# Kernel optimization log

Measured on AMD Instinct MI355X. Metric: run time of the kernel, lower is better.

The kernel has to match this reference:

```python
import jax, jax.numpy as jnp
import numpy as np

C = 64
C2 = C // 2


def conv1x1(x, w, b):
    # x: [B,Cin,H,W], w: [Cout,Cin], b: [Cout]
    return jnp.einsum('bchw,oc->bohw', x, w) + b[None, :, None, None]


def maxpool2(x):
    # 2x2 max pool, stride 2. x: [B,C,H,W] -> [B,C,H//2,W//2]
    B, Ch, H, W = x.shape
    x = x.reshape(B, Ch, H // 2, 2, W // 2, 2)
    return x.max(axis=(3, 5))


def setup_inputs() -> dict:
    key = jax.random.key(0)
    ks = jax.random.split(key, 9)
    B, H, W = 4, 128, 128
    x = jax.random.normal(ks[0], (B, C, H, W), dtype=jnp.float32)
    s_in = 1.0 / np.sqrt(C)
    s_mid = 1.0 / np.sqrt(C2)
    return {
        'x': x,
        'w_theta': jax.random.uniform(ks[1], (C2, C), jnp.float32, -s_in, s_in),
        'b_theta': jax.random.uniform(ks[2], (C2,), jnp.float32, -s_in, s_in),
        'w_phi': jax.random.uniform(ks[3], (C2, C), jnp.float32, -s_in, s_in),
        'b_phi': jax.random.uniform(ks[4], (C2,), jnp.float32, -s_in, s_in),
        'w_g': jax.random.uniform(ks[5], (C2, C), jnp.float32, -s_in, s_in),
        'b_g': jax.random.uniform(ks[6], (C2,), jnp.float32, -s_in, s_in),
        'w_out': jax.random.uniform(ks[7], (C, C2), jnp.float32, -s_mid, s_mid),
        'b_out': jax.random.uniform(ks[8], (C,), jnp.float32, -s_mid, s_mid),
    }


def reference(x, w_theta, b_theta, w_phi, b_phi, w_g, b_g, w_out, b_out):
    B, Ch, H, W = x.shape
    theta = conv1x1(x, w_theta, b_theta)            # [B,C2,H,W]
    phi = maxpool2(conv1x1(x, w_phi, b_phi))        # [B,C2,H/2,W/2]
    g = maxpool2(conv1x1(x, w_g, b_g))              # [B,C2,H/2,W/2]

    theta_flat = theta.reshape(B, C2, H * W).transpose(0, 2, 1)   # [B,HW,C2]
    phi_flat = phi.reshape(B, C2, -1)                              # [B,C2,hw4]
    g_flat = g.reshape(B, C2, -1).transpose(0, 2, 1)               # [B,hw4,C2]

    attn = jnp.einsum('bnc,bcm->bnm', theta_flat, phi_flat)       # [B,HW,hw4]
    attn = jax.nn.softmax(attn, axis=-1)
    y = jnp.einsum('bnm,bmc->bnc', attn, g_flat)                   # [B,HW,C2]
    y = y.transpose(0, 2, 1).reshape(B, C2, H, W)
    return conv1x1(y, w_out, b_out) + x
```

## Files before the change

kernel.cpp:

```cpp
#include <hip/hip_runtime.h>

#define HW    16384
#define Wh    128
#define Cin   64
#define C2    32
#define HW4   4096

typedef short short8 __attribute__((ext_vector_type(8)));
typedef float float4v __attribute__((ext_vector_type(4)));
typedef unsigned uint4v __attribute__((ext_vector_type(4)));

#define LOG2E 1.44269504f
#define OFFE  43.2808512f

__device__ __forceinline__ unsigned pack2bf16(float lo, float hi) {
  unsigned ul = __builtin_bit_cast(unsigned, lo);
  unsigned uh = __builtin_bit_cast(unsigned, hi);
  ul = (ul + 0x7fffu + ((ul >> 16) & 1u)) >> 16;
  uh = (uh + 0x7fffu + ((uh >> 16) & 1u)) & 0xffff0000u;
  return ul | uh;
}
__device__ __forceinline__ unsigned short f2bf(float f) {
  unsigned u = __builtin_bit_cast(unsigned, f);
  return (unsigned short)((u + 0x7fffu + ((u >> 16) & 1u)) >> 16);
}
__device__ __forceinline__ unsigned packtrunc(float lo, float hi) {
  return __builtin_amdgcn_perm(__builtin_bit_cast(unsigned, hi),
                               __builtin_bit_cast(unsigned, lo), 0x07060302u);
}

__global__ __launch_bounds__(256) void repack_w_kern(
    const float* __restrict__ wt, const float* __restrict__ bt,
    const float* __restrict__ wp, const float* __restrict__ bp,
    const float* __restrict__ wg, const float* __restrict__ bg,
    float* __restrict__ wAll, float* __restrict__ bAll) {
  int idx = blockIdx.x * 256 + threadIdx.x;
  if (idx < 6144) {
    int og = idx / 1536, rem = idx % 1536;
    int c = rem / 24, j = rem % 24;
    int o = og * 8 + (j & 7);
    float v;
    if (j < 8)       v = wt[o * Cin + c] * LOG2E;
    else if (j < 16) v = wp[o * Cin + c];
    else             v = wg[o * Cin + c];
    wAll[idx] = v;
  } else if (idx < 6240) {
    int i2 = idx - 6144;
    int og = i2 / 24, j = i2 % 24;
    int o = og * 8 + (j & 7);
    bAll[i2] = (j < 8) ? bt[o] * LOG2E : (j < 16 ? bp[o] : bg[o]);
  }
}

__global__ __launch_bounds__(256) void conv_qkv_kern(
    const float* __restrict__ x, const float* __restrict__ wAll,
    const float* __restrict__ bAll, unsigned short* __restrict__ Q,
    unsigned short* __restrict__ K, unsigned short* __restrict__ Vt) {
  __shared__ float smX[2][8][256];
  __shared__ unsigned short smV[8][64];
  int tid = threadIdx.x;
  int og = blockIdx.y, bz = blockIdx.z;
  int pxbase = blockIdx.x * 2 * Wh;
  int jloc = tid >> 2;
  int rpar = (tid >> 1) & 1, cpar = tid & 1;
  int myPx = rpar * Wh + 2 * jloc + cpar;
  const float* xb = x + (size_t)bz * Cin * HW + pxbase;
  const float* wc = wAll + og * 1536;
  const float* bb = bAll + og * 24;

  auto stage = [&](int cb8, int buf) {
#pragma unroll
    for (int u = 0; u < 2; ++u) {
      int f = u * 256 + tid;
      int ch = f >> 6, p4 = f & 63;
      *(float4*)&smX[buf][ch][p4 * 4] =
          *(const float4*)(xb + (size_t)(cb8 * 8 + ch) * HW + p4 * 4);
    }
  };

  float acc[24];
#pragma unroll
  for (int k = 0; k < 24; ++k) acc[k] = bb[k];

  stage(0, 0);
  __syncthreads();
  for (int cb8 = 0; cb8 < 8; ++cb8) {
    if (cb8 < 7) stage(cb8 + 1, (cb8 + 1) & 1);
    float xv[8];
#pragma unroll
    for (int u = 0; u < 8; ++u) xv[u] = smX[cb8 & 1][u][myPx];
#pragma unroll
    for (int u = 0; u < 8; ++u) {
#pragma unroll
      for (int k = 0; k < 24; ++k)
        acc[k] = fmaf(wc[(cb8 * 8 + u) * 24 + k], xv[u], acc[k]);
    }
    __syncthreads();
  }

  int pp = blockIdx.x * 64 + jloc;
  int p = pxbase + myPx;
  {
    uint4 up;
    up.x = pack2bf16(acc[0], acc[1]); up.y = pack2bf16(acc[2], acc[3]);
    up.z = pack2bf16(acc[4], acc[5]); up.w = pack2bf16(acc[6], acc[7]);
    *(uint4*)(Q + ((size_t)bz * HW + p) * C2 + og * 8) = up;
  }
  float aP[8], aG[8];
#pragma unroll
  for (int o = 0; o < 8; ++o) {
    float vp = acc[8 + o], vg = acc[16 + o];
    vp = fmaxf(vp, __shfl_xor(vp, 1)); vp = fmaxf(vp, __shfl_xor(vp, 2));
    vg = fmaxf(vg, __shfl_xor(vg, 1)); vg = fmaxf(vg, __shfl_xor(vg, 2));
    aP[o] = vp; aG[o] = vg;
  }
  if ((tid & 3) == 0) {
    int loc = pp & 31, tile = pp >> 5;
    int prow = ((loc & 4) << 2) + ((loc >> 3) << 2) + (loc & 3);
    uint4 up;
    up.x = pack2bf16(aP[0], aP[1]); up.y = pack2bf16(aP[2], aP[3]);
    up.z = pack2bf16(aP[4], aP[5]); up.w = pack2bf16(aP[6], aP[7]);
    *(uint4*)(K + ((size_t)bz * HW4 + tile * 32 + prow) * C2 + og * 8) = up;
#pragma unroll
    for (int o = 0; o < 8; ++o) smV[o][tid >> 2] = f2bf(aG[o]);
  }
  __syncthreads();
  {
    int ch = tid >> 5, idx = tid & 31;
    unsigned v = ((unsigned*)smV)[ch * 32 + idx];
    int tile = blockIdx.x * 2 + (idx >> 4);
    int kin = (2 * idx) & 31;
    *(unsigned*)(Vt + (size_t)bz * C2 * HW4 + (size_t)tile * (C2 * 32) +
                 (size_t)(og * 8 + ch) * 32 + kin) = v;
  }
}

__global__ __launch_bounds__(256, 4) void attn_mfma_kern(
    const unsigned short* __restrict__ Qb, const unsigned short* __restrict__ Kb,
    const unsigned short* __restrict__ Vt, float* __restrict__ Y) {
  __shared__ float smY[3][64][33];
  __shared__ float smL[4][64];
  int lane = threadIdx.x & 63;
  int wv = threadIdx.x >> 6;
  int quad = lane >> 4, l16 = lane & 15;
  int bz = blockIdx.y;
  int qrow0 = blockIdx.x * 64;

  short8 qf[4];
#pragma unroll
  for (int f = 0; f < 4; ++f)
    qf[f] = *(const short8*)(Qb + ((size_t)bz * HW + qrow0 + f * 16 + l16) * C2 + quad * 8);
  const unsigned short* kb = Kb + ((size_t)bz * HW4 + wv * 1024) * C2;
  const unsigned short* vb = Vt + (size_t)bz * C2 * HW4 + (size_t)(wv * 32) * 1024;

  short8 ones;
#pragma unroll
  for (int i = 0; i < 8; ++i) ones[i] = (short)0x3F80;

  float4v z = {0.f, 0.f, 0.f, 0.f};
  float4v ya[4] = {z, z, z, z};
  float4v yh[4] = {z, z, z, z};
  float4v y2[4] = {z, z, z, z};
  float4v moff = {-OFFE, -OFFE, -OFFE, -OFFE};

  for (int t = 0; t < 32; ++t) {
    const unsigned short* kt = kb + (size_t)t * 32 * C2;
    const unsigned short* vt = vb + (size_t)t * 1024;
    short8 ka = *(const short8*)(kt + (size_t)l16 * C2 + quad * 8);
    short8 kh = *(const short8*)(kt + (size_t)(16 + l16) * C2 + quad * 8);
    short8 va = *(const short8*)(vt + l16 * 32 + quad * 8);
    short8 vh = *(const short8*)(vt + (16 + l16) * 32 + quad * 8);
#pragma unroll
    for (int f = 0; f < 4; ++f) {
      float4v sa = __builtin_amdgcn_mfma_f32_16x16x32_bf16(ka, qf[f], moff, 0, 0, 0);
      float4v sh = __builtin_amdgcn_mfma_f32_16x16x32_bf16(kh, qf[f], moff, 0, 0, 0);
      float e0 = __builtin_amdgcn_exp2f(sa[0]), e1 = __builtin_amdgcn_exp2f(sa[1]);
      float e2 = __builtin_amdgcn_exp2f(sa[2]), e3 = __builtin_amdgcn_exp2f(sa[3]);
      float g0 = __builtin_amdgcn_exp2f(sh[0]), g1 = __builtin_amdgcn_exp2f(sh[1]);
      float g2 = __builtin_amdgcn_exp2f(sh[2]), g3 = __builtin_amdgcn_exp2f(sh[3]);
      uint4v d = {packtrunc(e0, e1), packtrunc(e2, e3),
                  packtrunc(g0, g1), packtrunc(g2, g3)};
      short8 pf = __builtin_bit_cast(short8, d);
      ya[f] = __builtin_amdgcn_mfma_f32_16x16x32_bf16(pf, va,   ya[f], 0, 0, 0);
      yh[f] = __builtin_amdgcn_mfma_f32_16x16x32_bf16(pf, vh,   yh[f], 0, 0, 0);
      y2[f] = __builtin_amdgcn_mfma_f32_16x16x32_bf16(pf, ones, y2[f], 0, 0, 0);
    }
  }

  if (l16 == 0) {
#pragma unroll
    for (int f = 0; f < 4; ++f)
#pragma unroll
      for (int r = 0; r < 4; ++r)
        smL[wv][f * 16 + quad * 4 + r] = y2[f][r];
  }
  if (wv > 0) {
    int pi = wv - 1;
#pragma unroll
    for (int f = 0; f < 4; ++f)
#pragma unroll
      for (int r = 0; r < 4; ++r) {
        int lr = f * 16 + quad * 4 + r;
        smY[pi][lr][l16] = ya[f][r];
        smY[pi][lr][16 + l16] = yh[f][r];
      }
  }
  __syncthreads();
  if (wv == 0) {
#pragma unroll
    for (int f = 0; f < 4; ++f)
#pragma unroll
      for (int r = 0; r < 4; ++r) {
        int lr = f * 16 + quad * 4 + r;
        float a0 = ya[f][r] + smY[0][lr][l16] + smY[1][lr][l16] + smY[2][lr][l16];
        float a1 = yh[f][r] + smY[0][lr][16 + l16] + smY[1][lr][16 + l16] + smY[2][lr][16 + l16];
        float L = smL[0][lr] + smL[1][lr] + smL[2][lr] + smL[3][lr];
        float inv = 1.f / L;
        size_t rw = (size_t)bz * HW + qrow0 + lr;
        Y[rw * C2 + l16] = a0 * inv;
        Y[rw * C2 + 16 + l16] = a1 * inv;
      }
  }
}

__global__ __launch_bounds__(256) void conv_out_kern(
    const float* __restrict__ Y, const float* __restrict__ x,
    const float* __restrict__ w, const float* __restrict__ bias,
    float* __restrict__ out) {
  int p = blockIdx.x * 256 + threadIdx.x;
  int cog = blockIdx.y, bz = blockIdx.z;
  const float* xb = x + (size_t)bz * Cin * HW + p;
  float xr[8];
#pragma unroll
  for (int i = 0; i < 8; ++i)
    xr[i] = xb[(size_t)(cog * 8 + i) * HW];
  float y[C2];
  const float4* yp4 = (const float4*)(Y + ((size_t)bz * HW + p) * C2);
#pragma unroll
  for (int i = 0; i < 8; ++i) {
    float4 t = yp4[i];
    y[4 * i] = t.x; y[4 * i + 1] = t.y; y[4 * i + 2] = t.z; y[4 * i + 3] = t.w;
  }
  float* ob = out + (size_t)bz * Cin * HW + p;
#pragma unroll
  for (int i = 0; i < 8; ++i) {
    int co = cog * 8 + i;
    float s = bias[co];
#pragma unroll
    for (int o = 0; o < C2; ++o) s = fmaf(w[co * C2 + o], y[o], s);
    ob[(size_t)co * HW] = s + xr[i];
  }
}

extern "C" void kernel_launch(void* const* d_in, const int* in_sizes, int n_in,
                              void* d_out, int out_size, void* d_ws, size_t ws_size,
                              hipStream_t stream) {
  const float* x       = (const float*)d_in[0];
  const float* w_theta = (const float*)d_in[1];
  const float* b_theta = (const float*)d_in[2];
  const float* w_phi   = (const float*)d_in[3];
  const float* b_phi   = (const float*)d_in[4];
  const float* w_g     = (const float*)d_in[5];
  const float* b_g     = (const float*)d_in[6];
  const float* w_out   = (const float*)d_in[7];
  const float* b_out   = (const float*)d_in[8];
  float* out = (float*)d_out;

  float* Yws = (float*)d_ws;
  unsigned short* Qb = (unsigned short*)(Yws + (size_t)4 * HW * C2);
  unsigned short* Kb = Qb + (size_t)4 * HW * C2;
  unsigned short* Vt = Kb + (size_t)4 * HW4 * C2;
  float* wAll = (float*)(Vt + (size_t)4 * HW4 * C2);
  float* bAll = wAll + 6144;

  repack_w_kern<<<25, 256, 0, stream>>>(w_theta, b_theta, w_phi, b_phi,
                                        w_g, b_g, wAll, bAll);
  conv_qkv_kern<<<dim3(64, 4, 4), 256, 0, stream>>>(x, wAll, bAll, Qb, Kb, Vt);
  attn_mfma_kern<<<dim3(HW / 64, 4), 256, 0, stream>>>(Qb, Kb, Vt, Yws);
  conv_out_kern<<<dim3(64, 8, 4), 256, 0, stream>>>(Yws, x, w_out, b_out, out);
}
```

Before: 152.2 us.

## Split attention key range across 8 waves with tree reduction

The attention kernel now launches 512 threads per block, so 8 waves each process 512 keys instead of 4 waves each processing 1024. This halves each wave's serial loop length and adds more waves per CU to hide MFMA and exp latency. Partial outputs are combined with a three-stage shared-memory tree reduction. The cost is extra barriers and LDS traffic, plus register pressure under the launch bound of 512 threads with 4 blocks.

```diff
diff --git a/kernel.cpp b/kernel.cpp
--- a/kernel.cpp
+++ b/kernel.cpp
@@ -135,11 +135,11 @@
   }
 }
 
-__global__ __launch_bounds__(256, 4) void attn_mfma_kern(
+__global__ __launch_bounds__(512, 4) void attn_mfma_kern(
     const unsigned short* __restrict__ Qb, const unsigned short* __restrict__ Kb,
     const unsigned short* __restrict__ Vt, float* __restrict__ Y) {
-  __shared__ float smY[3][64][33];
-  __shared__ float smL[4][64];
+  __shared__ float smY[4][64][33];
+  __shared__ float smL[8][64];
   int lane = threadIdx.x & 63;
   int wv = threadIdx.x >> 6;
   int quad = lane >> 4, l16 = lane & 15;
@@ -150,8 +150,8 @@
 #pragma unroll
   for (int f = 0; f < 4; ++f)
     qf[f] = *(const short8*)(Qb + ((size_t)bz * HW + qrow0 + f * 16 + l16) * C2 + quad * 8);
-  const unsigned short* kb = Kb + ((size_t)bz * HW4 + wv * 1024) * C2;
-  const unsigned short* vb = Vt + (size_t)bz * C2 * HW4 + (size_t)(wv * 32) * 1024;
+  const unsigned short* kb = Kb + ((size_t)bz * HW4 + wv * 512) * C2;
+  const unsigned short* vb = Vt + (size_t)bz * C2 * HW4 + (size_t)(wv * 16) * 1024;
 
   short8 ones;
 #pragma unroll
@@ -163,7 +163,7 @@
   float4v y2[4] = {z, z, z, z};
   float4v moff = {-OFFE, -OFFE, -OFFE, -OFFE};
 
-  for (int t = 0; t < 32; ++t) {
+  for (int t = 0; t < 16; ++t) {
     const unsigned short* kt = kb + (size_t)t * 32 * C2;
     const unsigned short* vt = vb + (size_t)t * 1024;
     short8 ka = *(const short8*)(kt + (size_t)l16 * C2 + quad * 8);
@@ -194,15 +194,58 @@
       for (int r = 0; r < 4; ++r)
         smL[wv][f * 16 + quad * 4 + r] = y2[f][r];
   }
-  if (wv > 0) {
-    int pi = wv - 1;
-#pragma unroll
-    for (int f = 0; f < 4; ++f)
-#pragma unroll
-      for (int r = 0; r < 4; ++r) {
-        int lr = f * 16 + quad * 4 + r;
-        smY[pi][lr][l16] = ya[f][r];
-        smY[pi][lr][16 + l16] = yh[f][r];
+  if (wv >= 4) {
+#pragma unroll
+    for (int f = 0; f < 4; ++f)
+#pragma unroll
+      for (int r = 0; r < 4; ++r) {
+        int lr = f * 16 + quad * 4 + r;
+        smY[wv - 4][lr][l16] = ya[f][r];
+        smY[wv - 4][lr][16 + l16] = yh[f][r];
+      }
+  }
+  __syncthreads();
+  if (wv < 4) {
+#pragma unroll
+    for (int f = 0; f < 4; ++f)
+#pragma unroll
+      for (int r = 0; r < 4; ++r) {
+        int lr = f * 16 + quad * 4 + r;
+        ya[f][r] += smY[wv][lr][l16];
+        yh[f][r] += smY[wv][lr][16 + l16];
+      }
+  }
+  __syncthreads();
+  if (wv == 2 || wv == 3) {
+#pragma unroll
+    for (int f = 0; f < 4; ++f)
+#pragma unroll
+      for (int r = 0; r < 4; ++r) {
+        int lr = f * 16 + quad * 4 + r;
+        smY[wv - 2][lr][l16] = ya[f][r];
+        smY[wv - 2][lr][16 + l16] = yh[f][r];
+      }
+  }
+  __syncthreads();
+  if (wv < 2) {
+#pragma unroll
+    for (int f = 0; f < 4; ++f)
+#pragma unroll
+      for (int r = 0; r < 4; ++r) {
+        int lr = f * 16 + quad * 4 + r;
+        ya[f][r] += smY[wv][lr][l16];
+        yh[f][r] += smY[wv][lr][16 + l16];
+      }
+  }
+  __syncthreads();
+  if (wv == 1) {
+#pragma unroll
+    for (int f = 0; f < 4; ++f)
+#pragma unroll
+      for (int r = 0; r < 4; ++r) {
+        int lr = f * 16 + quad * 4 + r;
+        smY[0][lr][l16] = ya[f][r];
+        smY[0][lr][16 + l16] = yh[f][r];
       }
   }
   __syncthreads();
@@ -212,9 +255,10 @@
 #pragma unroll
       for (int r = 0; r < 4; ++r) {
         int lr = f * 16 + quad * 4 + r;
-        float a0 = ya[f][r] + smY[0][lr][l16] + smY[1][lr][l16] + smY[2][lr][l16];
-        float a1 = yh[f][r] + smY[0][lr][16 + l16] + smY[1][lr][16 + l16] + smY[2][lr][16 + l16];
-        float L = smL[0][lr] + smL[1][lr] + smL[2][lr] + smL[3][lr];
+        float a0 = ya[f][r] + smY[0][lr][l16];
+        float a1 = yh[f][r] + smY[0][lr][16 + l16];
+        float L = smL[0][lr] + smL[1][lr] + smL[2][lr] + smL[3][lr] +
+                  smL[4][lr] + smL[5][lr] + smL[6][lr] + smL[7][lr];
         float inv = 1.f / L;
         size_t rw = (size_t)bz * HW + qrow0 + lr;
         Y[rw * C2 + l16] = a0 * inv;
@@ -276,6 +320,6 @@
   repack_w_kern<<<25, 256, 0, stream>>>(w_theta, b_theta, w_phi, b_phi,
                                         w_g, b_g, wAll, bAll);
   conv_qkv_kern<<<dim3(64, 4, 4), 256, 0, stream>>>(x, wAll, bAll, Qb, Kb, Vt);
-  attn_mfma_kern<<<dim3(HW / 64, 4), 256, 0, stream>>>(Qb, Kb, Vt, Yws);
+  attn_mfma_kern<<<dim3(HW / 64, 4), 512, 0, stream>>>(Qb, Kb, Vt, Yws);
   conv_out_kern<<<dim3(64, 8, 4), 256, 0, stream>>>(Yws, x, w_out, b_out, out);
 }
```

Measured after the change: 152.8 us. Within noise of the previous version (+0.4%).
